# Kernel optimization log

Hardware: AMD Instinct MI355X
Metric: run time of the kernel (lower is better)

The kernel has to match this reference:

```python
import jax, jax.numpy as jnp
import numpy as np

B, S, HID = 2, 2048, 2048
NH, NKV = 16, 4
HD = HID // NH            # 128
N_REP = NH // NKV          # 4
THETA = 10000.0
NEG = -1e9


def _rope_tables(position_ids):
    # inv_freq: [HD/2]
    inv_freq = 1.0 / (THETA ** (jnp.arange(0, HD, 2, dtype=jnp.float32) / HD))
    freqs = position_ids.astype(jnp.float32)[..., None] * inv_freq  # [B,S,HD/2]
    emb = jnp.concatenate([freqs, freqs], axis=-1)                  # [B,S,HD]
    return jnp.cos(emb), jnp.sin(emb)


def _rotate_half(x):
    return jnp.concatenate([-x[..., HD // 2:], x[..., :HD // 2]], axis=-1)


def setup_inputs() -> dict:
    key = jax.random.key(0)
    k1, k2, k3 = jax.random.split(key, 3)
    hidden_states = jax.random.normal(k1, (B, S, HID), dtype=jnp.float32)
    w_qkv = jax.random.normal(k2, (HID + 2 * NKV * HD, HID), dtype=jnp.float32) * 0.02
    w_out = jax.random.normal(k3, (HID, HID), dtype=jnp.float32) * 0.02
    causal = jnp.tril(jnp.ones((S, S), dtype=bool))
    attention_mask = jnp.where(causal, 0.0, NEG).astype(jnp.float32)
    attention_mask = jnp.broadcast_to(attention_mask[None, None], (B, 1, S, S))
    position_ids = jnp.broadcast_to(jnp.arange(S, dtype=jnp.int64), (B, S))
    return {"hidden_states": hidden_states, "w_qkv": w_qkv, "w_out": w_out,
            "attention_mask": attention_mask, "position_ids": position_ids}


def reference(hidden_states, w_qkv, w_out, attention_mask, position_ids):
    bsz, q_len, _ = hidden_states.shape
    qkv = hidden_states @ w_qkv.T                                   # [B,S,HID+2*NKV*HD]
    q, k, v = jnp.split(qkv, [HID, HID + NKV * HD], axis=-1)
    q = q.reshape(bsz, q_len, NH, HD).transpose(0, 2, 1, 3)         # [B,NH,S,HD]
    k = k.reshape(bsz, q_len, NKV, HD).transpose(0, 2, 1, 3)        # [B,NKV,S,HD]
    v = v.reshape(bsz, q_len, NKV, HD).transpose(0, 2, 1, 3)

    cos, sin = _rope_tables(position_ids)                           # [B,S,HD]
    cos, sin = cos[:, None], sin[:, None]                           # unsqueeze head dim
    q = q * cos + _rotate_half(q) * sin
    k = k * cos + _rotate_half(k) * sin

    # GQA: repeat KV heads to match query heads (repeat_kv)
    k = jnp.repeat(k, N_REP, axis=1)                                # [B,NH,S,HD]
    v = jnp.repeat(v, N_REP, axis=1)

    scale = 1.0 / jnp.sqrt(jnp.float32(HD))
    scores = jnp.einsum('bhqd,bhkd->bhqk', q, k) * scale
    scores = scores + attention_mask                                # [B,NH,S,S]
    attn = jax.nn.softmax(scores.astype(jnp.float32), axis=-1).astype(q.dtype)
    out = jnp.einsum('bhqk,bhkd->bhqd', attn, v)                    # [B,NH,S,HD]
    out = out.transpose(0, 2, 1, 3).reshape(bsz, q_len, HID)
    return out @ w_out.T
```

## Files before the change

kernel.cpp:

```cpp
#include <hip/hip_runtime.h>
#include <hip/hip_bf16.h>
#include <math.h>

#define S_LEN   2048
#define HIDDEN  2048
#define NHEADS  16
#define NKVH    4
#define HDIM    128

typedef short  short8  __attribute__((ext_vector_type(8)));
typedef float  floatx4 __attribute__((ext_vector_type(4)));
typedef __hip_bfloat16 bf16;

__device__ inline void async_copy16(const void* g, void* l) {
  __builtin_amdgcn_global_load_lds((__attribute__((address_space(1))) void*)(g),
                                   (__attribute__((address_space(3))) void*)(l),
                                   16, 0, 0);
}

__device__ inline unsigned short cvt1(float x) {
  bf16 t = __float2bfloat16(x);
  return *reinterpret_cast<unsigned short*>(&t);
}
__device__ inline float us2f(unsigned short u) {
  unsigned int v = ((unsigned int)u) << 16;
  return *reinterpret_cast<float*>(&v);
}

#define N8_H  1048576
#define N8_WQ  786432
#define N8_WO  524288
__global__ __launch_bounds__(256) void cvt_all(const float* __restrict__ h,
                                               const float* __restrict__ wq,
                                               const float* __restrict__ wo,
                                               unsigned short* __restrict__ dst) {
  const int i = blockIdx.x * 256 + threadIdx.x;
  if (i >= N8_H + N8_WQ + N8_WO) return;
  const float* src; int j;
  if (i < N8_H)              { src = h;  j = i; }
  else if (i < N8_H + N8_WQ) { src = wq; j = i - N8_H; }
  else                       { src = wo; j = i - N8_H - N8_WQ; }
  const float4 a = reinterpret_cast<const float4*>(src)[j * 2];
  const float4 b = reinterpret_cast<const float4*>(src)[j * 2 + 1];
  unsigned short o[8] = {cvt1(a.x), cvt1(a.y), cvt1(a.z), cvt1(a.w),
                         cvt1(b.x), cvt1(b.y), cvt1(b.z), cvt1(b.w)};
  *reinterpret_cast<short8*>(dst + (size_t)i * 8) = *reinterpret_cast<short8*>(o);
}

template<int MODE>
__global__ __launch_bounds__(256) void gemm_bt(const bf16* __restrict__ A,
                                               const bf16* __restrict__ B,
                                               int M, int N, int K,
                                               bf16* __restrict__ qbuf,
                                               bf16* __restrict__ kbuf,
                                               bf16* __restrict__ vtbuf,
                                               float* __restrict__ Cout)
{
  __shared__ unsigned short As[128 * 32];
  __shared__ unsigned short Bs[128 * 32];
  const int t    = threadIdx.x;
  const int w    = t >> 6;
  const int lane = t & 63;
  const int m16  = lane & 15;
  const int quad = lane >> 4;
  const int wm   = (w >> 1) * 64;
  const int wn   = (w & 1) * 64;
  const int bm   = blockIdx.y, bn = blockIdx.x;

  int bcol[4];
#pragma unroll
  for (int ni = 0; ni < 4; ++ni)
    bcol[ni] = (MODE == 0) ? ((w & 1) * 32 + (ni & 1) * 16 + (ni >> 1) * 64)
                           : (wn + ni * 16);

  const floatx4 zf = {0.f, 0.f, 0.f, 0.f};
  floatx4 acc[4][4];
#pragma unroll
  for (int i = 0; i < 4; ++i)
#pragma unroll
    for (int j = 0; j < 4; ++j) acc[i][j] = zf;

  const bf16* gA = A + (size_t)(bm * 128 + (t >> 2)) * K + (t & 3) * 8;
  const bf16* gB = B + (size_t)(bn * 128 + (t >> 2)) * K + (t & 3) * 8;
  unsigned short* lA = &As[w * 512];
  unsigned short* lB = &Bs[w * 512];

  for (int k0 = 0; k0 < K; k0 += 32) {
    __syncthreads();
#pragma unroll
    for (int i = 0; i < 2; ++i) {
      async_copy16(gA + (size_t)(64 * i) * K + k0, lA + i * 2048);
      async_copy16(gB + (size_t)(64 * i) * K + k0, lB + i * 2048);
    }
    __builtin_amdgcn_s_waitcnt(0);
    __syncthreads();
    short8 af[4], bfr[4];
#pragma unroll
    for (int mi = 0; mi < 4; ++mi)
      af[mi] = *reinterpret_cast<const short8*>(&As[(wm + mi * 16 + m16) * 32 + quad * 8]);
#pragma unroll
    for (int ni = 0; ni < 4; ++ni)
      bfr[ni] = *reinterpret_cast<const short8*>(&Bs[(bcol[ni] + m16) * 32 + quad * 8]);
#pragma unroll
    for (int mi = 0; mi < 4; ++mi)
#pragma unroll
      for (int ni = 0; ni < 4; ++ni)
        acc[mi][ni] = __builtin_amdgcn_mfma_f32_16x16x32_bf16(af[mi], bfr[ni], acc[mi][ni], 0, 0, 0);
  }

  if (MODE == 1) {
#pragma unroll
    for (int mi = 0; mi < 4; ++mi)
#pragma unroll
      for (int ni = 0; ni < 4; ++ni) {
        const int row0 = bm * 128 + wm + mi * 16 + quad * 4;
        const int col  = bn * 128 + bcol[ni] + m16;
#pragma unroll
        for (int r = 0; r < 4; ++r)
          Cout[(size_t)(row0 + r) * N + col] = acc[mi][ni][r];
      }
    return;
  }

  const int colbase = bn * 128;
  if (colbase < HIDDEN + NKVH * HDIM) {
    const bool isQ = (colbase < HIDDEN);
    const float post = isQ ? 0.08838834764831845f : 1.0f;
    float invf[2];
#pragma unroll
    for (int p = 0; p < 2; ++p)
      invf[p] = exp2f((float)((w & 1) * 32 + p * 16 + m16) * -0.2076205059f);
#pragma unroll
    for (int mi = 0; mi < 4; ++mi) {
      const int row0 = bm * 128 + wm + mi * 16 + quad * 4;
#pragma unroll
      for (int r = 0; r < 4; ++r) {
        const int m = row0 + r;
        const int b = m >> 11, s = m & 2047;
        float sn[2], cs[2];
        __sincosf((float)s * invf[0], &sn[0], &cs[0]);
        __sincosf((float)s * invf[1], &sn[1], &cs[1]);
#pragma unroll
        for (int ni = 0; ni < 4; ++ni) {
          const int p = ni & 1;
          const float v  = acc[mi][ni][r];
          const float v2 = acc[mi][ni ^ 2][r];
          const float rot = ((ni < 2) ? (v * cs[p] - v2 * sn[p])
                                      : (v * cs[p] + v2 * sn[p])) * post;
          const int col = colbase + bcol[ni] + m16;
          if (isQ) {
            const int hh = col >> 7, d = col & 127;
            qbuf[(((size_t)(b * NHEADS + hh)) * S_LEN + s) * HDIM + d] = __float2bfloat16(rot);
          } else {
            const int nn = col - HIDDEN; const int hh = nn >> 7, d = nn & 127;
            kbuf[(((size_t)(b * NKVH + hh)) * S_LEN + s) * HDIM + d] = __float2bfloat16(rot);
          }
        }
      }
    }
  } else {
#pragma unroll
    for (int mi = 0; mi < 4; ++mi)
#pragma unroll
      for (int ni = 0; ni < 4; ++ni) {
        const int row0 = bm * 128 + wm + mi * 16 + quad * 4;
        const int col  = colbase + bcol[ni] + m16;
        const int nn = col - HIDDEN - NKVH * HDIM;
        const int hh = nn >> 7, d = nn & 127;
#pragma unroll
        for (int r = 0; r < 4; ++r) {
          const int m = row0 + r;
          const int b = m >> 11, s = m & 2047;
          vtbuf[(((size_t)(b * NKVH + hh)) * HDIM + d) * S_LEN + s] =
              __float2bfloat16(acc[mi][ni][r]);
        }
      }
  }
}

__global__ __launch_bounds__(256) void attn_partial(const bf16* __restrict__ qbuf,
                                                    const bf16* __restrict__ kbuf,
                                                    const bf16* __restrict__ vtbuf,
                                                    unsigned short* __restrict__ pnum,
                                                    float* __restrict__ plsum)
{
  __shared__ unsigned short Ks[2][4096];
  __shared__ unsigned short Vs[2][4096];
  __shared__ unsigned short Ps[4][1280];
  const int sidx = 110 - blockIdx.x;
  int i2, c, nch;
  if (sidx < 27)      { i2 = sidx;                     c = 0;              nch = 1; }
  else if (sidx < 81) { i2 = 27 + ((sidx - 27) >> 1);  c = (sidx - 27) & 1; nch = 2; }
  else                { i2 = 54 + (sidx - 81) / 3;     c = (sidx - 81) % 3; nch = 3; }
  const int len = i2 + 1;
  const int k0 = (c * len) / nch, k1 = ((c + 1) * len) / nch;
  const int kvh = blockIdx.y, b = blockIdx.z;
  const int t = threadIdx.x, w = t >> 6, lane = t & 63;
  const int m16 = lane & 15, quad = lane >> 4;
  const int h = kvh * 4 + w;

  const bf16* Qp = qbuf + (((size_t)(b * NHEADS + h)) * S_LEN + i2 * 32 + m16) * HDIM;
  short8 qf[2][4];
#pragma unroll
  for (int T = 0; T < 2; ++T)
#pragma unroll
    for (int cc = 0; cc < 4; ++cc)
      qf[T][cc] = *reinterpret_cast<const short8*>(Qp + (size_t)T * 16 * HDIM + cc * 32 + quad * 8);

  const bf16* Kp  = kbuf  + ((size_t)(b * NKVH + kvh)) * S_LEN * HDIM;
  const bf16* Vtp = vtbuf + ((size_t)(b * NKVH + kvh)) * HDIM * S_LEN;

  const int kk = lane >> 4, cK = lane & 15;
  const int rKa = w * 8 + kk, rKb = rKa + 4;
  const int offKa = rKa * 128 + ((cK ^ (rKa & 7)) * 8);
  const int offKb = rKb * 128 + ((cK ^ (rKb & 7)) * 8);
  const int dd = lane >> 2, cV = lane & 3;
  const int dVa = w * 32 + dd, dVb = dVa + 16;
  const int offVa = dVa * 2048 + ((cV ^ ((dVa >> 1) & 3)) * 8);
  const int offVb = dVb * 2048 + ((cV ^ ((dVb >> 1) & 3)) * 8);

  const floatx4 zf = {0.f, 0.f, 0.f, 0.f};
  floatx4 oacc[2][8];
#pragma unroll
  for (int T = 0; T < 2; ++T)
#pragma unroll
    for (int d = 0; d < 8; ++d) oacc[T][d] = zf;
  floatx4 lacc[2] = {zf, zf};
  unsigned short ones_s[8] = {0x3F80,0x3F80,0x3F80,0x3F80,0x3F80,0x3F80,0x3F80,0x3F80};
  const short8 ones = *reinterpret_cast<short8*>(ones_s);

  unsigned short* Pw = &Ps[w][0];

  {
    const int ks = k0 * 32;
    async_copy16(Kp + (size_t)ks * 128 + offKa, &Ks[0][w * 1024]);
    async_copy16(Kp + (size_t)ks * 128 + offKb, &Ks[0][w * 1024 + 512]);
    async_copy16(Vtp + ks + offVa, &Vs[0][w * 1024]);
    async_copy16(Vtp + ks + offVb, &Vs[0][w * 1024 + 512]);
  }
  __syncthreads();

  for (int ki = k0; ki < k1; ++ki) {
    const int buf = (ki - k0) & 1;
    if (ki + 1 < k1) {
      const int ks = (ki + 1) * 32;
      async_copy16(Kp + (size_t)ks * 128 + offKa, &Ks[buf ^ 1][w * 1024]);
      async_copy16(Kp + (size_t)ks * 128 + offKb, &Ks[buf ^ 1][w * 1024 + 512]);
      async_copy16(Vtp + ks + offVa, &Vs[buf ^ 1][w * 1024]);
      async_copy16(Vtp + ks + offVb, &Vs[buf ^ 1][w * 1024 + 512]);
    }
    const int ks = ki * 32;
    floatx4 s00 = zf, s01 = zf, s10 = zf, s11 = zf;
#pragma unroll
    for (int cc = 0; cc < 4; ++cc) {
      const int sw = ((cc * 4 + quad) ^ (m16 & 7)) * 8;
      short8 kf0 = *reinterpret_cast<const short8*>(&Ks[buf][m16 * 128 + sw]);
      short8 kf1 = *reinterpret_cast<const short8*>(&Ks[buf][(16 + m16) * 128 + sw]);
      s00 = __builtin_amdgcn_mfma_f32_16x16x32_bf16(qf[0][cc], kf0, s00, 0, 0, 0);
      s01 = __builtin_amdgcn_mfma_f32_16x16x32_bf16(qf[0][cc], kf1, s01, 0, 0, 0);
      s10 = __builtin_amdgcn_mfma_f32_16x16x32_bf16(qf[1][cc], kf0, s10, 0, 0, 0);
      s11 = __builtin_amdgcn_mfma_f32_16x16x32_bf16(qf[1][cc], kf1, s11, 0, 0, 0);
    }
#pragma unroll
    for (int T = 0; T < 2; ++T) {
      const floatx4& sa = T ? s10 : s00;
      const floatx4& sb = T ? s11 : s01;
#pragma unroll
      for (int r = 0; r < 4; ++r) {
        const int row = i2 * 32 + T * 16 + quad * 4 + r;
        const float p0 = (ks + m16      > row) ? 0.f : __expf(sa[r]);
        const float p1 = (ks + 16 + m16 > row) ? 0.f : __expf(sb[r]);
        Pw[(T * 16 + quad * 4 + r) * 40 + m16]      = cvt1(p0);
        Pw[(T * 16 + quad * 4 + r) * 40 + 16 + m16] = cvt1(p1);
      }
    }
    const short8 pa0 = *reinterpret_cast<const short8*>(&Pw[m16 * 40 + quad * 8]);
    const short8 pa1 = *reinterpret_cast<const short8*>(&Pw[(16 + m16) * 40 + quad * 8]);
    lacc[0] = __builtin_amdgcn_mfma_f32_16x16x32_bf16(pa0, ones, lacc[0], 0, 0, 0);
    lacc[1] = __builtin_amdgcn_mfma_f32_16x16x32_bf16(pa1, ones, lacc[1], 0, 0, 0);
#pragma unroll
    for (int dt = 0; dt < 8; ++dt) {
      short8 vfr = *reinterpret_cast<const short8*>(
          &Vs[buf][(dt * 16 + m16) * 32 + ((quad ^ ((m16 >> 1) & 3)) * 8)]);
      oacc[0][dt] = __builtin_amdgcn_mfma_f32_16x16x32_bf16(pa0, vfr, oacc[0][dt], 0, 0, 0);
      oacc[1][dt] = __builtin_amdgcn_mfma_f32_16x16x32_bf16(pa1, vfr, oacc[1][dt], 0, 0, 0);
    }
    __syncthreads();
  }

  const int b0 = (i2 < 27) ? i2 : ((i2 < 54) ? (27 + 2 * (i2 - 27)) : (81 + 3 * (i2 - 54)));
  const int slot = (b * NHEADS + h) * 111 + b0 + c;
  unsigned short* np = pnum + (size_t)slot * 4096;
#pragma unroll
  for (int T = 0; T < 2; ++T)
#pragma unroll
    for (int dt = 0; dt < 8; ++dt)
#pragma unroll
      for (int r = 0; r < 4; ++r)
        np[(T * 16 + quad * 4 + r) * 128 + dt * 16 + m16] = cvt1(oacc[T][dt][r]);
  if (m16 == 0) {
#pragma unroll
    for (int T = 0; T < 2; ++T)
#pragma unroll
      for (int r = 0; r < 4; ++r)
        plsum[slot * 32 + T * 16 + quad * 4 + r] = lacc[T][r];
  }
}

__global__ __launch_bounds__(256) void attn_combine(const unsigned short* __restrict__ pnum,
                                                    const float* __restrict__ plsum,
                                                    bf16* __restrict__ abuf)
{
  const int i = blockIdx.x, h = blockIdx.y, b = blockIdx.z;
  const int i2 = i >> 1, lr0 = (i & 1) * 16;
  const int t = threadIdx.x, row16 = t >> 4, c0 = (t & 15) * 8;
  const int lr = lr0 + row16;
  const int nch = (i2 < 27) ? 1 : ((i2 < 54) ? 2 : 3);
  const int b0  = (i2 < 27) ? i2 : ((i2 < 54) ? (27 + 2 * (i2 - 27)) : (81 + 3 * (i2 - 54)));
  const int hb = (b * NHEADS + h) * 111 + b0;
  float acc[8] = {0.f,0.f,0.f,0.f,0.f,0.f,0.f,0.f};
  float lsum = 0.f;
  for (int c = 0; c < nch; ++c) {
    const unsigned short* np = pnum + (size_t)(hb + c) * 4096 + lr * 128 + c0;
    const short8 v = *reinterpret_cast<const short8*>(np);
#pragma unroll
    for (int j = 0; j < 8; ++j) acc[j] += us2f(((unsigned short*)&v)[j]);
    lsum += plsum[(hb + c) * 32 + lr];
  }
  const float invl = 1.0f / lsum;
  unsigned short o[8];
#pragma unroll
  for (int j = 0; j < 8; ++j) o[j] = cvt1(acc[j] * invl);
  *reinterpret_cast<short8*>(abuf + (((size_t)b * S_LEN + i * 16 + row16) * NHEADS + h) * HDIM + c0)
      = *reinterpret_cast<short8*>(o);
}

extern "C" void kernel_launch(void* const* d_in, const int* in_sizes, int n_in,
                              void* d_out, int out_size, void* d_ws, size_t ws_size,
                              hipStream_t stream) {
  const float* hidden_f = (const float*)d_in[0];
  const float* wqkv_f   = (const float*)d_in[1];
  const float* wout_f   = (const float*)d_in[2];
  float* out = (float*)d_out;

  char* ws = (char*)d_ws;
  bf16* hbf    = (bf16*)(ws);
  bf16* wqkvbf = (bf16*)(ws + 16777216);
  bf16* woutbf = (bf16*)(ws + 29360128);
  bf16* qbuf   = (bf16*)(ws + 37748736);
  bf16* kbuf   = (bf16*)(ws + 54525952);
  bf16* vtbuf  = (bf16*)(ws + 58720256);
  bf16* abuf   = (bf16*)(ws + 62914560);
  unsigned short* pnum = (unsigned short*)(ws);
  float* plsum = (float*)(ws + 79691776);

  cvt_all<<<9216, 256, 0, stream>>>(hidden_f, wqkv_f, wout_f, (unsigned short*)ws);

  gemm_bt<0><<<dim3(24, 32), 256, 0, stream>>>(hbf, wqkvbf, 4096, 3072, 2048,
                                               qbuf, kbuf, vtbuf, nullptr);
  attn_partial<<<dim3(111, 4, 2), 256, 0, stream>>>(qbuf, kbuf, vtbuf, pnum, plsum);
  attn_combine<<<dim3(128, 16, 2), 256, 0, stream>>>(pnum, plsum, abuf);
  gemm_bt<1><<<dim3(16, 32), 256, 0, stream>>>(abuf, woutbf, 4096, 2048, 2048,
                                               nullptr, nullptr, nullptr, out);
}
```

Before: 339.2 us.

## Precompute RoPE table, remap GEMM blocks per XCD, finalize single-chunk attention directly

Three independent changes. A small kernel precomputes a cos/sin table, which the QKV GEMM epilogue reads instead of evaluating sincos per element. Both GEMMs switch to a 1D grid that assigns a contiguous group of N-tiles to each XCD, aiming at better L2 reuse of B tiles. Attention blocks that cover a whole row block (one chunk) now normalize and write their output straight to abuf, so the combine kernel only runs over the split rows. The costs are an extra kernel launch and table memory traffic in place of cheap sincos math.

Result: slower. 367.8 us (+8.4%).

```diff
diff --git a/kernel.cpp b/kernel.cpp
--- a/kernel.cpp
+++ b/kernel.cpp
@@ -25,6 +25,15 @@
 __device__ inline float us2f(unsigned short u) {
   unsigned int v = ((unsigned int)u) << 16;
   return *reinterpret_cast<float*>(&v);
+}
+
+__global__ __launch_bounds__(256) void rope_table(float2* __restrict__ rt) {
+  const int i = blockIdx.x * 256 + threadIdx.x;
+  const int s = i >> 6, j = i & 63;
+  const float inv = exp2f((float)j * -0.2076205059f);
+  float sn, cs;
+  __sincosf((float)s * inv, &sn, &cs);
+  rt[i] = make_float2(cs, sn);
 }
 
 #define N8_H  1048576
@@ -50,7 +59,8 @@
 template<int MODE>
 __global__ __launch_bounds__(256) void gemm_bt(const bf16* __restrict__ A,
                                                const bf16* __restrict__ B,
-                                               int M, int N, int K,
+                                               int M, int N, int K, int bng,
+                                               const float2* __restrict__ rtab,
                                                bf16* __restrict__ qbuf,
                                                bf16* __restrict__ kbuf,
                                                bf16* __restrict__ vtbuf,
@@ -58,6 +68,10 @@
 {
   __shared__ unsigned short As[128 * 32];
   __shared__ unsigned short Bs[128 * 32];
+  const int id   = blockIdx.x;
+  const int xcd  = id & 7, jj = id >> 3;
+  const int bn   = xcd * bng + (jj % bng);
+  const int bm   = jj / bng;
   const int t    = threadIdx.x;
   const int w    = t >> 6;
   const int lane = t & 63;
@@ -65,7 +79,6 @@
   const int quad = lane >> 4;
   const int wm   = (w >> 1) * 64;
   const int wn   = (w & 1) * 64;
-  const int bm   = blockIdx.y, bn = blockIdx.x;
 
   int bcol[4];
 #pragma unroll
@@ -126,10 +139,7 @@
   if (colbase < HIDDEN + NKVH * HDIM) {
     const bool isQ = (colbase < HIDDEN);
     const float post = isQ ? 0.08838834764831845f : 1.0f;
-    float invf[2];
-#pragma unroll
-    for (int p = 0; p < 2; ++p)
-      invf[p] = exp2f((float)((w & 1) * 32 + p * 16 + m16) * -0.2076205059f);
+    const int jbase = (w & 1) * 32 + m16;
 #pragma unroll
     for (int mi = 0; mi < 4; ++mi) {
       const int row0 = bm * 128 + wm + mi * 16 + quad * 4;
@@ -137,16 +147,17 @@
       for (int r = 0; r < 4; ++r) {
         const int m = row0 + r;
         const int b = m >> 11, s = m & 2047;
-        float sn[2], cs[2];
-        __sincosf((float)s * invf[0], &sn[0], &cs[0]);
-        __sincosf((float)s * invf[1], &sn[1], &cs[1]);
+        const float2 t0 = rtab[(s << 6) + jbase];
+        const float2 t1 = rtab[(s << 6) + jbase + 16];
+        const float csv[2] = {t0.x, t1.x};
+        const float snv[2] = {t0.y, t1.y};
 #pragma unroll
         for (int ni = 0; ni < 4; ++ni) {
           const int p = ni & 1;
           const float v  = acc[mi][ni][r];
           const float v2 = acc[mi][ni ^ 2][r];
-          const float rot = ((ni < 2) ? (v * cs[p] - v2 * sn[p])
-                                      : (v * cs[p] + v2 * sn[p])) * post;
+          const float rot = ((ni < 2) ? (v * csv[p] - v2 * snv[p])
+                                      : (v * csv[p] + v2 * snv[p])) * post;
           const int col = colbase + bcol[ni] + m16;
           if (isQ) {
             const int hh = col >> 7, d = col & 127;
@@ -182,7 +193,8 @@
                                                     const bf16* __restrict__ kbuf,
                                                     const bf16* __restrict__ vtbuf,
                                                     unsigned short* __restrict__ pnum,
-                                                    float* __restrict__ plsum)
+                                                    float* __restrict__ plsum,
+                                                    bf16* __restrict__ abuf)
 {
   __shared__ unsigned short Ks[2][4096];
   __shared__ unsigned short Vs[2][4096];
@@ -288,22 +300,37 @@
     __syncthreads();
   }
 
-  const int b0 = (i2 < 27) ? i2 : ((i2 < 54) ? (27 + 2 * (i2 - 27)) : (81 + 3 * (i2 - 54)));
-  const int slot = (b * NHEADS + h) * 111 + b0 + c;
-  unsigned short* np = pnum + (size_t)slot * 4096;
-#pragma unroll
-  for (int T = 0; T < 2; ++T)
-#pragma unroll
-    for (int dt = 0; dt < 8; ++dt)
-#pragma unroll
-      for (int r = 0; r < 4; ++r)
-        np[(T * 16 + quad * 4 + r) * 128 + dt * 16 + m16] = cvt1(oacc[T][dt][r]);
-  if (m16 == 0) {
+  if (nch == 1) {
+#pragma unroll
+    for (int T = 0; T < 2; ++T) {
+      float invl[4];
+#pragma unroll
+      for (int r = 0; r < 4; ++r) invl[r] = 1.0f / lacc[T][r];
+      bf16* op = abuf + (((size_t)b * S_LEN + i2 * 32 + T * 16 + quad * 4) * NHEADS + h) * HDIM + m16;
+#pragma unroll
+      for (int dt = 0; dt < 8; ++dt)
+#pragma unroll
+        for (int r = 0; r < 4; ++r)
+          op[(size_t)r * NHEADS * HDIM + dt * 16] = __float2bfloat16(oacc[T][dt][r] * invl[r]);
+    }
+  } else {
+    const int b0 = (i2 < 54) ? (27 + 2 * (i2 - 27)) : (81 + 3 * (i2 - 54));
+    const int slot = (b * NHEADS + h) * 111 + b0 + c;
+    unsigned short* np = pnum + (size_t)slot * 4096;
 #pragma unroll
     for (int T = 0; T < 2; ++T)
 #pragma unroll
-      for (int r = 0; r < 4; ++r)
-        plsum[slot * 32 + T * 16 + quad * 4 + r] = lacc[T][r];
+      for (int dt = 0; dt < 8; ++dt)
+#pragma unroll
+        for (int r = 0; r < 4; ++r)
+          np[(T * 16 + quad * 4 + r) * 128 + dt * 16 + m16] = cvt1(oacc[T][dt][r]);
+    if (m16 == 0) {
+#pragma unroll
+      for (int T = 0; T < 2; ++T)
+#pragma unroll
+        for (int r = 0; r < 4; ++r)
+          plsum[slot * 32 + T * 16 + quad * 4 + r] = lacc[T][r];
+    }
   }
 }
 
@@ -311,12 +338,13 @@
                                                     const float* __restrict__ plsum,
                                                     bf16* __restrict__ abuf)
 {
-  const int i = blockIdx.x, h = blockIdx.y, b = blockIdx.z;
+  const int i = 54 + blockIdx.x;
+  const int h = blockIdx.y, b = blockIdx.z;
   const int i2 = i >> 1, lr0 = (i & 1) * 16;
   const int t = threadIdx.x, row16 = t >> 4, c0 = (t & 15) * 8;
   const int lr = lr0 + row16;
-  const int nch = (i2 < 27) ? 1 : ((i2 < 54) ? 2 : 3);
-  const int b0  = (i2 < 27) ? i2 : ((i2 < 54) ? (27 + 2 * (i2 - 27)) : (81 + 3 * (i2 - 54)));
+  const int nch = (i2 < 54) ? 2 : 3;
+  const int b0  = (i2 < 54) ? (27 + 2 * (i2 - 27)) : (81 + 3 * (i2 - 54));
   const int hb = (b * NHEADS + h) * 111 + b0;
   float acc[8] = {0.f,0.f,0.f,0.f,0.f,0.f,0.f,0.f};
   float lsum = 0.f;
@@ -353,13 +381,15 @@
   bf16* abuf   = (bf16*)(ws + 62914560);
   unsigned short* pnum = (unsigned short*)(ws);
   float* plsum = (float*)(ws + 79691776);
-
+  float2* rtab = (float2*)(ws + 81788928);
+
+  rope_table<<<512, 256, 0, stream>>>(rtab);
   cvt_all<<<9216, 256, 0, stream>>>(hidden_f, wqkv_f, wout_f, (unsigned short*)ws);
 
-  gemm_bt<0><<<dim3(24, 32), 256, 0, stream>>>(hbf, wqkvbf, 4096, 3072, 2048,
-                                               qbuf, kbuf, vtbuf, nullptr);
-  attn_partial<<<dim3(111, 4, 2), 256, 0, stream>>>(qbuf, kbuf, vtbuf, pnum, plsum);
-  attn_combine<<<dim3(128, 16, 2), 256, 0, stream>>>(pnum, plsum, abuf);
-  gemm_bt<1><<<dim3(16, 32), 256, 0, stream>>>(abuf, woutbf, 4096, 2048, 2048,
-                                               nullptr, nullptr, nullptr, out);
-}
+  gemm_bt<0><<<768, 256, 0, stream>>>(hbf, wqkvbf, 4096, 3072, 2048, 3, rtab,
+                                      qbuf, kbuf, vtbuf, nullptr);
+  attn_partial<<<dim3(111, 4, 2), 256, 0, stream>>>(qbuf, kbuf, vtbuf, pnum, plsum, abuf);
+  attn_combine<<<dim3(74, 16, 2), 256, 0, stream>>>(pnum, plsum, abuf);
+  gemm_bt<1><<<512, 256, 0, stream>>>(abuf, woutbf, 4096, 2048, 2048, 2, nullptr,
+                                      nullptr, nullptr, nullptr, out);
+}
```
